# Performance work log

Hardware: AMD Instinct MI355X
Metric: run time of the kernel (lower is better)

## Reference

```python
import jax, jax.numpy as jnp
import numpy as np

BER = 0.02          # ber_curve.ber_at(snr_db) evaluated at snr_db=10
BITS = 9            # ceil(log2(512)) for both coarse and fine codebooks
KC = 512
KF = 512
B, HC, WC, HF, WF, D = 64, 32, 32, 64, 64, 128


def _bitflip_channel(idx, u, bits, K):
    """Pack->bitflip->unpack->clip, vectorized.

    LSB-first packing of exactly bits-per-symbol means flipping bits of the
    packed byte stream == flipping each symbol's `bits` bits independently
    (flipped padding bits in the final byte are discarded by unpack).
    idx: [...] int32, u: [..., bits] float32 uniform(0,1).
    """
    shifts = jnp.arange(bits, dtype=jnp.int32)
    bitmat = (idx[..., None] >> shifts) & 1                       # [..., bits]
    flips = (u < BER).astype(jnp.int32)
    bitmat = jnp.bitwise_xor(bitmat, flips)
    rx = jnp.sum(bitmat << shifts, axis=-1)                       # [...]
    return jnp.clip(rx, 0, K - 1)


def setup_inputs() -> dict:
    key = jax.random.key(0)
    k1, k2, k3, k4, k5, k6 = jax.random.split(key, 6)
    return {
        "idx_c": jax.random.randint(k1, (B, HC, WC), 0, KC, dtype=jnp.int32),
        "idx_f": jax.random.randint(k2, (B, HF, WF), 0, KF, dtype=jnp.int32),
        "codebook_c": jax.random.normal(k3, (KC, D), dtype=jnp.float32),
        "codebook_f": jax.random.normal(k4, (KF, D), dtype=jnp.float32),
        "flip_u_c": jax.random.uniform(k5, (B, HC, WC, BITS), dtype=jnp.float32),
        "flip_u_f": jax.random.uniform(k6, (B, HF, WF, BITS), dtype=jnp.float32),
    }


def reference(idx_c, idx_f, codebook_c, codebook_f, flip_u_c, flip_u_f):
    rx_c = _bitflip_channel(idx_c, flip_u_c, BITS, KC)            # [B,Hc,Wc]
    rx_f = _bitflip_channel(idx_f, flip_u_f, BITS, KF)            # [B,Hf,Wf]
    # indices_to_quantized: embedding gather from each codebook
    q_coarse = codebook_c[rx_c]                                   # [B,Hc,Wc,D]
    q_fine = codebook_f[rx_f]                                     # [B,Hf,Wf,D]
    b = q_fine.shape[0]
    out = jnp.concatenate(
        [q_fine.reshape(b, -1), q_coarse.reshape(b, -1)], axis=1
    )
    return out
```

## Files before the change

### kernel.cpp

```cpp
#include <hip/hip_runtime.h>


constexpr int   BITS       = 9;
constexpr float BER        = 0.02f;
constexpr int   Bn         = 64;
constexpr int   HC = 32, WC = 32, HF = 64, WF = 64, D = 128;
constexpr int   NF         = Bn * HF * WF;
constexpr int   NC         = Bn * HC * WC;
constexpr int   NTOT       = NF + NC;
constexpr int   FINE_ROW   = HF * WF * D;
constexpr int   COARSE_ROW = HC * WC * D;
constexpr int   ROW        = FINE_ROW + COARSE_ROW;

constexpr int   GRID  = 2048;
constexpr int   SYMS_PER_BLK_ITER = 8;
constexpr int   ITERS = NTOT / (SYMS_PER_BLK_ITER * GRID);

__global__ __launch_bounds__(256) void chan_gather_kernel(
    const int*   __restrict__ idx_c,
    const int*   __restrict__ idx_f,
    const float* __restrict__ cb_c,
    const float* __restrict__ cb_f,
    const float* __restrict__ u_c,
    const float* __restrict__ u_f,
    float*       __restrict__ out)
{
    const int t          = threadIdx.x;
    const int sym_in_blk = t >> 5;
    const int half       = (t >> 5) & 1;
    const int lane32     = t & 31;

    #pragma unroll
    for (int it = 0; it < ITERS; ++it) {
        const int c = it * GRID + blockIdx.x;
        const int i = c * SYMS_PER_BLK_ITER + sym_in_blk;

        const float* u;  const int* idxp;  const float* cb;
        int off, local;
        if (i < NF) {
            const int b = i >> 12, rem = i & 4095;
            off   = b * ROW + rem * D;
            u     = u_f;  idxp = idx_f;  cb = cb_f;
            local = i;
        } else {
            const int j = i - NF;
            const int b = j >> 10, rem = j & 1023;
            off   = b * ROW + FINE_ROW + rem * D;
            u     = u_c;  idxp = idx_c;  cb = cb_c;
            local = j;
        }

        bool pred = false;
        if (lane32 < BITS)
            pred = u[(size_t)local * BITS + lane32] < BER;
        const unsigned long long m = __ballot(pred);
        const int flip = (int)((m >> (half << 5)) & 511u);

        const int row = (idxp[local] ^ flip) & 511;

        const float4 val = ((const float4*)(cb + row * D))[lane32];
        ((float4*)(out + off))[lane32] = val;
    }
}

extern "C" void kernel_launch(void* const* d_in, const int* in_sizes, int n_in,
                              void* d_out, int out_size, void* d_ws, size_t ws_size,
                              hipStream_t stream) {
    const int*   idx_c = (const int*)  d_in[0];
    const int*   idx_f = (const int*)  d_in[1];
    const float* cb_c  = (const float*)d_in[2];
    const float* cb_f  = (const float*)d_in[3];
    const float* u_c   = (const float*)d_in[4];
    const float* u_f   = (const float*)d_in[5];
    float*       out   = (float*)d_out;

    chan_gather_kernel<<<GRID, 256, 0, stream>>>(
        idx_c, idx_f, cb_c, cb_f, u_c, u_f, out);
}
```

Before: 204.3 us.

## Split bit-flip decoding into a separate kernel before the codebook gather

Moves the bit-flip channel computation into its own kernel, where each thread decodes one symbol and writes the received index to workspace. The gather kernel then only reads the precomputed row index and copies the codebook row, with no ballot or dependent flip-probability loads on its critical path. The unroll in the gather loop drops from full to 2. In exchange it adds a second launch and a round trip through the workspace for the index array, and the flip kernel reads the uniforms with strided per-thread loads.

New measurement: 184.5 us. 9.7% less time.

```diff
diff --git a/kernel.cpp b/kernel.cpp
--- a/kernel.cpp
+++ b/kernel.cpp
@@ -12,51 +12,52 @@
 constexpr int   COARSE_ROW = HC * WC * D;
 constexpr int   ROW        = FINE_ROW + COARSE_ROW;
 
-constexpr int   GRID  = 2048;
-constexpr int   SYMS_PER_BLK_ITER = 8;
-constexpr int   ITERS = NTOT / (SYMS_PER_BLK_ITER * GRID);
-
-__global__ __launch_bounds__(256) void chan_gather_kernel(
+__global__ __launch_bounds__(256) void flip_kernel(
     const int*   __restrict__ idx_c,
     const int*   __restrict__ idx_f,
+    const float* __restrict__ u_c,
+    const float* __restrict__ u_f,
+    int*         __restrict__ rx)
+{
+    const int s = blockIdx.x * 256 + threadIdx.x;
+    const float* u;  const int* idxp;  int local;
+    if (s < NF) { u = u_f; idxp = idx_f; local = s; }
+    else        { u = u_c; idxp = idx_c; local = s - NF; }
+    const float* up = u + (size_t)local * BITS;
+    int flip = 0;
+    #pragma unroll
+    for (int k = 0; k < BITS; ++k)
+        flip |= (up[k] < BER) ? (1 << k) : 0;
+    rx[s] = (idxp[local] ^ flip) & 511;
+}
+
+constexpr int GRID  = 2048;
+constexpr int ITERS = NTOT / (8 * GRID);
+
+__global__ __launch_bounds__(256) void gather_kernel(
     const float* __restrict__ cb_c,
     const float* __restrict__ cb_f,
-    const float* __restrict__ u_c,
-    const float* __restrict__ u_f,
+    const int*   __restrict__ rx,
     float*       __restrict__ out)
 {
     const int t          = threadIdx.x;
     const int sym_in_blk = t >> 5;
-    const int half       = (t >> 5) & 1;
     const int lane32     = t & 31;
 
-    #pragma unroll
+    #pragma unroll 2
     for (int it = 0; it < ITERS; ++it) {
-        const int c = it * GRID + blockIdx.x;
-        const int i = c * SYMS_PER_BLK_ITER + sym_in_blk;
+        const int i = (it * GRID + blockIdx.x) * 8 + sym_in_blk;
+        const int row = rx[i];
 
-        const float* u;  const int* idxp;  const float* cb;
-        int off, local;
+        const float* cb;  int off;
         if (i < NF) {
             const int b = i >> 12, rem = i & 4095;
-            off   = b * ROW + rem * D;
-            u     = u_f;  idxp = idx_f;  cb = cb_f;
-            local = i;
+            off = b * ROW + rem * D;                cb = cb_f;
         } else {
             const int j = i - NF;
             const int b = j >> 10, rem = j & 1023;
-            off   = b * ROW + FINE_ROW + rem * D;
-            u     = u_c;  idxp = idx_c;  cb = cb_c;
-            local = j;
+            off = b * ROW + FINE_ROW + rem * D;     cb = cb_c;
         }
-
-        bool pred = false;
-        if (lane32 < BITS)
-            pred = u[(size_t)local * BITS + lane32] < BER;
-        const unsigned long long m = __ballot(pred);
-        const int flip = (int)((m >> (half << 5)) & 511u);
-
-        const int row = (idxp[local] ^ flip) & 511;
 
         const float4 val = ((const float4*)(cb + row * D))[lane32];
         ((float4*)(out + off))[lane32] = val;
@@ -73,7 +74,8 @@
     const float* u_c   = (const float*)d_in[4];
     const float* u_f   = (const float*)d_in[5];
     float*       out   = (float*)d_out;
+    int*         rx    = (int*)d_ws;
 
-    chan_gather_kernel<<<GRID, 256, 0, stream>>>(
-        idx_c, idx_f, cb_c, cb_f, u_c, u_f, out);
+    flip_kernel<<<NTOT / 256, 256, 0, stream>>>(idx_c, idx_f, u_c, u_f, rx);
+    gather_kernel<<<GRID, 256, 0, stream>>>(cb_c, cb_f, rx, out);
 }
```
